# Optimization experiments

Hardware: AMD Instinct MI355X
Metric: run time of the kernel (lower is better)

## Reference

```python
import jax, jax.numpy as jnp
import numpy as np
from jax import lax

B = 64          # graphs per batch
N0 = 1024       # nodes per graph (equal-sized graphs -> static topk shapes)
DEG = 16        # avg degree
E = B * N0 * DEG
D_IN, D_H, D_OUT = 100, 128, 256
RATIO, EPS = 0.5, 1e-5


def _seg_sum(v, idx, n):
    return jax.ops.segment_sum(v, idx, num_segments=n)


def _gcn(x, src, dst, w_e, W, b, n):
    h = x @ W
    deg = 1.0 + _seg_sum(w_e, dst, n)          # +1 for self-loop
    dinv = lax.rsqrt(deg)
    norm = (dinv[src] * dinv[dst] * w_e)[:, None]
    return _seg_sum(h[src] * norm, dst, n) + h / deg[:, None] + b


def _graphnorm(x, w, bias, ms, nb, k):
    # PyG GraphNorm: per-graph mean/var with learnable mean_scale
    xg = x.reshape(nb, k, -1)
    mean = xg.mean(1, keepdims=True)
    sub = xg - ms * mean
    var = (sub * sub).mean(1, keepdims=True)
    return (w * sub * lax.rsqrt(var + EPS) + bias).reshape(nb * k, -1)


def _topk(x, src, dst, emask, p, nb, n_per):
    # TopKPooling (min_score=None): score = tanh(x.p/||p||), keep top ceil(r*n)
    k = int(np.ceil(RATIO * n_per))
    score = jnp.tanh((x @ p) / jnp.linalg.norm(p))
    vals, idx = lax.top_k(score.reshape(nb, n_per), k)            # [nb, k]
    perm = (idx + (jnp.arange(nb) * n_per)[:, None]).reshape(-1)
    x_new = x[perm] * vals.reshape(-1)[:, None]
    mapping = jnp.full((nb * n_per,), -1, jnp.int32).at[perm].set(
        jnp.arange(nb * k, dtype=jnp.int32))
    ns, nd = mapping[src], mapping[dst]
    valid = emask & (ns >= 0) & (nd >= 0)   # filter_adj as a persistent mask
    return x_new, jnp.where(valid, ns, 0), jnp.where(valid, nd, 0), valid, k


def _forward(x, edge_index, W1, b1, W2, b2, W3, b3,
             gn1_w, gn1_b, gn1_ms, gn2_w, gn2_b, gn2_ms,
             gn3_w, gn3_b, gn3_ms, p1, p2, p3):
    src, dst = edge_index[0], edge_index[1]
    emask = jnp.ones(src.shape, bool)
    Ws, bs = (W1, W2, W3), (b1, b2, b3)
    gw = (gn1_w, gn2_w, gn3_w)
    gb = (gn1_b, gn2_b, gn3_b)
    gm = (gn1_ms, gn2_ms, gn3_ms)
    ps = (p1, p2, p3)
    n_per = N0
    for i in range(3):
        n = B * n_per
        x = _gcn(x, src, dst, emask.astype(x.dtype), Ws[i], bs[i], n)
        x = _graphnorm(x, gw[i], gb[i], gm[i], B, n_per)
        x = jax.nn.relu(x)              # dropout: identity in eval mode
        x, src, dst, emask, n_per = _topk(x, src, dst, emask, ps[i], B, n_per)
    xg = x.reshape(B, n_per, D_OUT)
    # global mean/max pool then concat -> [B, 2*D_OUT]
    return jnp.concatenate([xg.mean(1), xg.max(1)], axis=1)


def setup_inputs():
    key = jax.random.key(0)
    ks = jax.random.split(key, 20)
    x = jax.random.normal(ks[0], (B * N0, D_IN), jnp.float32)
    # random edges within each graph, then offset by graph base index
    e = jax.random.randint(ks[1], (2, B, N0 * DEG), 0, N0, jnp.int32)
    edge_index = (e + (jnp.arange(B, dtype=jnp.int32) * N0)[None, :, None]).reshape(2, -1)
    batch = jnp.repeat(jnp.arange(B, dtype=jnp.int32), N0)
    inp = dict(x=x, edge_index=edge_index, batch=batch)
    dims = [(D_IN, D_H), (D_H, D_H), (D_H, D_OUT)]
    for i, (di, do) in enumerate(dims, 1):
        inp[f"W{i}"] = jax.random.normal(ks[1 + i], (di, do), jnp.float32) / np.sqrt(di)
        inp[f"b{i}"] = jnp.zeros((do,), jnp.float32)
        inp[f"gn{i}_w"] = jnp.ones((do,), jnp.float32)
        inp[f"gn{i}_b"] = jnp.zeros((do,), jnp.float32)
        inp[f"gn{i}_ms"] = jnp.ones((do,), jnp.float32)
        inp[f"p{i}"] = jax.random.normal(ks[10 + i], (do,), jnp.float32)
    return inp


def reference(x, edge_index, batch, W1, b1, W2, b2, W3, b3,
              gn1_w, gn1_b, gn1_ms, gn2_w, gn2_b, gn2_ms,
              gn3_w, gn3_b, gn3_ms, p1, p2, p3):
    del batch  # equal-sized graphs: grouping is encoded by constants B, N0
    return _forward(x, edge_index, W1, b1, W2, b2, W3, b3,
                    gn1_w, gn1_b, gn1_ms, gn2_w, gn2_b, gn2_ms,
                    gn3_w, gn3_b, gn3_ms, p1, p2, p3)
```

## Files before the change

### kernel.cpp

```cpp
#include <hip/hip_runtime.h>

#define GN_EPS 1e-5f

constexpr int NB   = 64;
constexpr int EPG  = 16384;
constexpr int ETOT = NB * EPG;
constexpr int NTOT = 64 * 1024;

__global__ void cmap_init_kernel(int* __restrict__ cmap) {
    int i = blockIdx.x * blockDim.x + threadIdx.x;
    if (i < NTOT) cmap[i] = i;
}

template <int NPG>
__global__ __launch_bounds__(1024) void csr_build_kernel(
        const int* __restrict__ ei, const int* __restrict__ cmap,
        int* __restrict__ cnt, int* __restrict__ offs, float* __restrict__ dinv,
        int2* __restrict__ csr_pack) {
    __shared__ int   lcnt[NPG];
    __shared__ float sdv[NPG];
    __shared__ int   wsum[16];
    constexpr int NW = NPG / 64;
    const int g = blockIdx.x;
    const int t = threadIdx.x;
    const int ebase = g * EPG;
    constexpr int EPT = EPG / 1024;

    for (int i = t; i < NPG; i += 1024) lcnt[i] = 0;
    __syncthreads();

    int ms_[EPT], md_[EPT];
#pragma unroll
    for (int i = 0; i < EPT; i++) {
        int e = ebase + t + i * 1024;
        int s = cmap[ei[e]];
        int d = cmap[ei[ETOT + e]];
        bool ok = (s >= 0) && (d >= 0);
        ms_[i] = ok ? s : -1;
        md_[i] = ok ? (d - g * NPG) : 0;
        if (ok) atomicAdd(&lcnt[d - g * NPG], 1);
    }
    __syncthreads();

    const int lane = t & 63;
    const int wid  = t >> 6;
    int orig = (t < NPG) ? lcnt[t] : 0;
    int v = orig;
#pragma unroll
    for (int d = 1; d < 64; d <<= 1) {
        int u = __shfl_up(v, d);
        if (lane >= d) v += u;
    }
    if (lane == 63) wsum[wid] = v;
    __syncthreads();
    if (wid == 0) {
        int wv = (lane < NW) ? wsum[lane] : 0;
#pragma unroll
        for (int d = 1; d < 16; d <<= 1) {
            int u = __shfl_up(wv, d);
            if (lane >= d) wv += u;
        }
        if (lane < NW) wsum[lane] = wv;
    }
    __syncthreads();
    if (t < NPG) {
        int incl = v + ((wid > 0) ? wsum[wid - 1] : 0);
        int excl = incl - orig;
        float dv = rsqrtf(1.0f + (float)orig);
        cnt[g * NPG + t]  = orig;
        offs[g * NPG + t] = ebase + excl;
        dinv[g * NPG + t] = dv;
        sdv[t] = dv;
        lcnt[t] = excl;
    }
    __syncthreads();

#pragma unroll
    for (int i = 0; i < EPT; i++) {
        int s = ms_[i];
        if (s >= 0) {
            int pos = atomicAdd(&lcnt[md_[i]], 1);
            csr_pack[ebase + pos] = make_int2(s, __float_as_int(sdv[s - g * NPG]));
        }
    }
}

template <int D4>
__global__ __launch_bounds__(256) void gather_kernel(
        const float* __restrict__ x, const int* __restrict__ cnt,
        const int* __restrict__ offs, const float* __restrict__ dinv,
        const int2* __restrict__ csr_pack, float* __restrict__ z, int n, int bpg) {
    constexpr int GRP = 8;
    constexpr int NPB = 256 / GRP;
    constexpr int CPL = 4;
    int bid   = blockIdx.x;
    int xcd   = bid & 7;
    int slot  = bid >> 3;
    int graph = xcd + 8 * (slot / bpg);
    int local = slot % bpg;
    int vb    = graph * bpg + local;

    int grp  = threadIdx.x / GRP;
    int lane = threadIdx.x % GRP;
    int v = vb * NPB + grp;
    if (v >= n) return;

    const float4* x4 = reinterpret_cast<const float4*>(x);
    int st = offs[v];
    int c  = cnt[v];
    float dv = dinv[v];

    int f4_[CPL];
    bool act[CPL];
#pragma unroll
    for (int i = 0; i < CPL; i++) {
        f4_[i] = lane + GRP * i;
        act[i] = f4_[i] < D4;
    }

    float4 acc[CPL];
#pragma unroll
    for (int i = 0; i < CPL; i++) {
        if (act[i]) {
            float4 xv = x4[(size_t)v * D4 + f4_[i]];
            acc[i] = {xv.x * dv, xv.y * dv, xv.z * dv, xv.w * dv};
        } else {
            acc[i] = {0.f, 0.f, 0.f, 0.f};
        }
    }

    int j = 0;
    for (; j + 2 <= c; j += 2) {
        int2 p0 = csr_pack[st + j];
        int2 p1 = csr_pack[st + j + 1];
        float d0 = __int_as_float(p0.y);
        float d1 = __int_as_float(p1.y);
        size_t r0 = (size_t)p0.x * D4;
        size_t r1 = (size_t)p1.x * D4;
#pragma unroll
        for (int i = 0; i < CPL; i++) {
            if (!act[i]) continue;
            float4 h0 = x4[r0 + f4_[i]];
            float4 h1 = x4[r1 + f4_[i]];
            acc[i].x += h0.x * d0 + h1.x * d1;
            acc[i].y += h0.y * d0 + h1.y * d1;
            acc[i].z += h0.z * d0 + h1.z * d1;
            acc[i].w += h0.w * d0 + h1.w * d1;
        }
    }
    if (j < c) {
        int2 p0 = csr_pack[st + j];
        float d0 = __int_as_float(p0.y);
        size_t r0 = (size_t)p0.x * D4;
#pragma unroll
        for (int i = 0; i < CPL; i++) {
            if (!act[i]) continue;
            float4 h0 = x4[r0 + f4_[i]];
            acc[i].x += h0.x * d0; acc[i].y += h0.y * d0;
            acc[i].z += h0.z * d0; acc[i].w += h0.w * d0;
        }
    }
#pragma unroll
    for (int i = 0; i < CPL; i++) {
        if (!act[i]) continue;
        float4 o = {acc[i].x * dv, acc[i].y * dv, acc[i].z * dv, acc[i].w * dv};
        reinterpret_cast<float4*>(z)[(size_t)v * D4 + f4_[i]] = o;
    }
}

__global__ __launch_bounds__(256) void gemm128_kernel(const float* __restrict__ A,
                                                      const float* __restrict__ W,
                                                      const float* __restrict__ Bias,
                                                      float* __restrict__ C,
                                                      int M, int N, int K) {
    __shared__ float As[16][132];
    __shared__ float Bs[16][132];
    const int bm = blockIdx.x * 128;
    const int bn = blockIdx.y * 128;
    const int tid = threadIdx.x;
    const int tx = tid & 15, ty = tid >> 4;

    const int arow = tid >> 1;
    const int ak   = (tid & 1) * 8;
    const int brow = tid >> 5;
    const int bc4  = (tid & 31) * 4;

    float acc[2][2][4][4] = {};

    for (int k0 = 0; k0 < K; k0 += 16) {
        {
            const float* ap = A + (size_t)(bm + arow) * K + k0 + ak;
            float4 a0 = {0,0,0,0}, a1 = {0,0,0,0};
            if (k0 + ak < K)     a0 = *reinterpret_cast<const float4*>(ap);
            if (k0 + ak + 4 < K) a1 = *reinterpret_cast<const float4*>(ap + 4);
            As[ak + 0][arow] = a0.x; As[ak + 1][arow] = a0.y;
            As[ak + 2][arow] = a0.z; As[ak + 3][arow] = a0.w;
            As[ak + 4][arow] = a1.x; As[ak + 5][arow] = a1.y;
            As[ak + 6][arow] = a1.z; As[ak + 7][arow] = a1.w;
        }
        {
            float4 b0 = {0,0,0,0}, b1 = {0,0,0,0};
            if (k0 + brow < K)
                b0 = *reinterpret_cast<const float4*>(W + (size_t)(k0 + brow) * N + bn + bc4);
            if (k0 + brow + 8 < K)
                b1 = *reinterpret_cast<const float4*>(W + (size_t)(k0 + brow + 8) * N + bn + bc4);
            *reinterpret_cast<float4*>(&Bs[brow][bc4])     = b0;
            *reinterpret_cast<float4*>(&Bs[brow + 8][bc4]) = b1;
        }
        __syncthreads();
#pragma unroll
        for (int k = 0; k < 16; k++) {
            float4 a0 = *reinterpret_cast<const float4*>(&As[k][ty * 4]);
            float4 a1 = *reinterpret_cast<const float4*>(&As[k][64 + ty * 4]);
            float4 b0 = *reinterpret_cast<const float4*>(&Bs[k][tx * 4]);
            float4 b1 = *reinterpret_cast<const float4*>(&Bs[k][64 + tx * 4]);
            const float av[2][4] = {{a0.x, a0.y, a0.z, a0.w}, {a1.x, a1.y, a1.z, a1.w}};
            const float bv[2][4] = {{b0.x, b0.y, b0.z, b0.w}, {b1.x, b1.y, b1.z, b1.w}};
#pragma unroll
            for (int qi = 0; qi < 2; qi++)
#pragma unroll
                for (int qj = 0; qj < 2; qj++)
#pragma unroll
                    for (int i = 0; i < 4; i++)
#pragma unroll
                        for (int j = 0; j < 4; j++)
                            acc[qi][qj][i][j] += av[qi][i] * bv[qj][j];
        }
        __syncthreads();
    }
    float4 bb[2];
    bb[0] = *reinterpret_cast<const float4*>(&Bias[bn + tx * 4]);
    bb[1] = *reinterpret_cast<const float4*>(&Bias[bn + 64 + tx * 4]);
#pragma unroll
    for (int qi = 0; qi < 2; qi++)
#pragma unroll
        for (int i = 0; i < 4; i++) {
            int row = bm + qi * 64 + ty * 4 + i;
#pragma unroll
            for (int qj = 0; qj < 2; qj++) {
                float4 o = {acc[qi][qj][i][0] + bb[qj].x, acc[qi][qj][i][1] + bb[qj].y,
                            acc[qi][qj][i][2] + bb[qj].z, acc[qi][qj][i][3] + bb[qj].w};
                *reinterpret_cast<float4*>(&C[(size_t)row * N + bn + qj * 64 + tx * 4]) = o;
            }
        }
}

template <int D4>
__global__ __launch_bounds__(256) void gn_partial_kernel(
        const float* __restrict__ x, float* __restrict__ sum1, float* __restrict__ sum2,
        int n_per) {
    constexpr int GROUPS = 256 / D4;
    __shared__ float4 l1[256];
    __shared__ float4 l2[256];
    int g = blockIdx.x >> 3;
    int ch = blockIdx.x & 7;
    int f4 = threadIdx.x % D4;
    int grp = threadIdx.x / D4;
    int chunk = n_per / 8;
    int base = g * n_per + ch * chunk;
    const float4* x4 = reinterpret_cast<const float4*>(x);
    float4 s1 = {0.f, 0.f, 0.f, 0.f}, s2 = {0.f, 0.f, 0.f, 0.f};
    for (int i = grp; i < chunk; i += GROUPS) {
        float4 v = x4[(size_t)(base + i) * D4 + f4];
        s1.x += v.x; s1.y += v.y; s1.z += v.z; s1.w += v.w;
        s2.x += v.x * v.x; s2.y += v.y * v.y; s2.z += v.z * v.z; s2.w += v.w * v.w;
    }
    int t = threadIdx.x;
    l1[t] = s1; l2[t] = s2;
    __syncthreads();
    for (int str = 128; str >= D4; str >>= 1) {
        if (t < str) {
            float4 a = l1[t + str], b2 = l2[t + str];
            l1[t].x += a.x; l1[t].y += a.y; l1[t].z += a.z; l1[t].w += a.w;
            l2[t].x += b2.x; l2[t].y += b2.y; l2[t].z += b2.z; l2[t].w += b2.w;
        }
        __syncthreads();
    }
    if (t < D4) {
        size_t slot = (size_t)(g * 8 + ch) * (D4 * 4) + t * 4;
        *reinterpret_cast<float4*>(&sum1[slot]) = l1[t];
        *reinterpret_cast<float4*>(&sum2[slot]) = l2[t];
    }
}

__global__ void pnorm3_kernel(const float* __restrict__ p0, const float* __restrict__ p1,
                              const float* __restrict__ p2, int d0, int d1, int d2,
                              float* __restrict__ out) {
    __shared__ float red[256];
    const float* p = (blockIdx.x == 0) ? p0 : (blockIdx.x == 1) ? p1 : p2;
    int d          = (blockIdx.x == 0) ? d0 : (blockIdx.x == 1) ? d1 : d2;
    int t = threadIdx.x;
    float v = (t < d) ? p[t] : 0.0f;
    red[t] = v * v;
    __syncthreads();
    for (int s = 128; s; s >>= 1) {
        if (t < s) red[t] += red[t + s];
        __syncthreads();
    }
    if (t == 0) out[blockIdx.x] = 1.0f / sqrtf(red[0]);
}

template <int DO>
__global__ __launch_bounds__(256) void gn_apply_score_kernel(
        float* __restrict__ x, const float* __restrict__ sum1, const float* __restrict__ sum2,
        const float* __restrict__ ms, const float* __restrict__ w,
        const float* __restrict__ bias, const float* __restrict__ p,
        const float* __restrict__ pinv, float* __restrict__ score, int n_per) {
    constexpr int V = DO / 64;
    __shared__ float scm[DO];
    __shared__ float ssr[DO];
    int node = blockIdx.x * 4 + (threadIdx.x >> 6);
    int lane = threadIdx.x & 63;
    int g = node / n_per;
    float inv_n = 1.0f / (float)n_per;
    for (int f = threadIdx.x; f < DO; f += 256) {
        float s1 = 0.f, s2 = 0.f;
#pragma unroll
        for (int ch = 0; ch < 8; ch++) {
            s1 += sum1[(size_t)(g * 8 + ch) * DO + f];
            s2 += sum2[(size_t)(g * 8 + ch) * DO + f];
        }
        float mean = s1 * inv_n;
        float ex2  = s2 * inv_n;
        float m = ms[f];
        float var = ex2 - 2.f * m * mean * mean + m * m * mean * mean;
        scm[f] = m * mean;
        ssr[f] = w[f] * rsqrtf(var + GN_EPS);
    }
    __syncthreads();

    float*       xr = x + (size_t)node * DO + lane * V;
    const float* bb = bias + lane * V;
    const float* pp = p + lane * V;
    float dot = 0.f;
#pragma unroll
    for (int i = 0; i < V; i++) {
        int f = lane * V + i;
        float y = (xr[i] - scm[f]) * ssr[f] + bb[i];
        y = fmaxf(y, 0.0f);
        xr[i] = y;
        dot += y * pp[i];
    }
#pragma unroll
    for (int off = 32; off; off >>= 1) dot += __shfl_xor(dot, off);
    if (lane == 0) score[node] = tanhf(dot * pinv[0]);
}

template <int N, int K>
__global__ __launch_bounds__(1024) void topk_radix_kernel(
        const float* __restrict__ score, int* __restrict__ mapping,
        int* __restrict__ inv) {
    __shared__ int hist[256];
    __shared__ int sscan[N];
    __shared__ int sbyte, sneed;
    const int g = blockIdx.x;
    const int t = threadIdx.x;
    float sc = score[g * N + t];
    unsigned u = __float_as_uint(sc);
    unsigned key = (u & 0x80000000u) ? ~u : (u | 0x80000000u);

    unsigned prefix = 0;
    int need = K;
#pragma unroll
    for (int shift = 24; shift >= 0; shift -= 8) {
        if (t < 256) hist[t] = 0;
        __syncthreads();
        unsigned hm = (shift == 24) ? 0u : (0xFFFFFFFFu << (shift + 8));
        if ((key & hm) == (prefix & hm))
            atomicAdd(&hist[(key >> shift) & 255], 1);
        __syncthreads();
        if (t < 256) sscan[t] = hist[t];
        __syncthreads();
        for (int d = 1; d < 256; d <<= 1) {
            int x = (t < 256 && t + d < 256) ? sscan[t + d] : 0;
            __syncthreads();
            if (t < 256) sscan[t] += x;
            __syncthreads();
        }
        if (t < 256) {
            int ge  = sscan[t];
            int gt_ = (t + 1 < 256) ? sscan[t + 1] : 0;
            if (ge >= need && gt_ < need) { sbyte = t; sneed = need - gt_; }
        }
        __syncthreads();
        prefix |= ((unsigned)sbyte << shift);
        need = sneed;
        __syncthreads();
    }
    bool gt = key > prefix;
    bool eq = (key == prefix);
    sscan[t] = (gt ? (1 << 16) : 0) | (eq ? 1 : 0);
    __syncthreads();
    for (int d = 1; d < N; d <<= 1) {
        int x = (t >= d) ? sscan[t - d] : 0;
        __syncthreads();
        sscan[t] += x;
        __syncthreads();
    }
    int incl   = sscan[t];
    int gtrank = (incl >> 16) - (gt ? 1 : 0);
    int eqrank = (incl & 0xFFFF) - (eq ? 1 : 0);
    int cntGT  = K - need;
    bool sel = gt || (eq && (eqrank < need));
    int old_g = g * N + t;
    if (sel) {
        int slot = gt ? gtrank : (cntGT + eqrank);
        mapping[old_g] = g * K + slot;
        inv[g * K + slot] = old_g;
    } else {
        mapping[old_g] = -1;
    }
}

__global__ void permute_compose_kernel(const float* __restrict__ x, const int* __restrict__ inv,
                                       const float* __restrict__ score, float* __restrict__ xn,
                                       int total, int ldof4,
                                       int* __restrict__ cmap, const int* __restrict__ mapping) {
    int t = blockIdx.x * blockDim.x + threadIdx.x;
    if (t < total) {
        int node = t >> ldof4;
        int f4   = t & ((1 << ldof4) - 1);
        int dof4 = 1 << ldof4;
        int old = inv[node];
        float sc = score[old];
        float4 v = reinterpret_cast<const float4*>(x)[(size_t)old * dof4 + f4];
        float4 o = {v.x * sc, v.y * sc, v.z * sc, v.w * sc};
        reinterpret_cast<float4*>(xn)[t] = o;
    }
    if (t < NTOT) {
        int c = cmap[t];
        cmap[t] = (c >= 0) ? mapping[c] : -1;
    }
}

__global__ __launch_bounds__(1024) void pool_sel_kernel(const float* __restrict__ x,
                                                        const int* __restrict__ inv,
                                                        const float* __restrict__ score,
                                                        float* __restrict__ out) {
    __shared__ float ssum[1024];
    __shared__ float smax[1024];
    int g = blockIdx.x;
    int f = threadIdx.x & 255;
    int ch = threadIdx.x >> 8;
    float s = 0.f, mx = -INFINITY;
    for (int i = ch; i < 128; i += 4) {
        int old = inv[g * 128 + i];
        float sc = score[old];
        float v = x[(size_t)old * 256 + f] * sc;
        s += v;
        mx = fmaxf(mx, v);
    }
    ssum[threadIdx.x] = s;
    smax[threadIdx.x] = mx;
    __syncthreads();
    if (ch == 0) {
#pragma unroll
        for (int c = 1; c < 4; c++) {
            s  += ssum[f + c * 256];
            mx  = fmaxf(mx, smax[f + c * 256]);
        }
        out[g * 512 + f]       = s / 128.0f;
        out[g * 512 + 256 + f] = mx;
    }
}

static inline int cdiv_h(int a, int b) { return (a + b - 1) / b; }

extern "C" void kernel_launch(void* const* d_in, const int* in_sizes, int n_in,
                              void* d_out, int out_size, void* d_ws, size_t ws_size,
                              hipStream_t stream) {
    (void)in_sizes; (void)n_in; (void)out_size; (void)ws_size;

    const float* x_in = (const float*)d_in[0];
    const int*   ei   = (const int*)d_in[1];
    const float* Wm[3]  = {(const float*)d_in[3],  (const float*)d_in[9],  (const float*)d_in[15]};
    const float* bv[3]  = {(const float*)d_in[4],  (const float*)d_in[10], (const float*)d_in[16]};
    const float* gnw[3] = {(const float*)d_in[5],  (const float*)d_in[11], (const float*)d_in[17]};
    const float* gnb[3] = {(const float*)d_in[6],  (const float*)d_in[12], (const float*)d_in[18]};
    const float* gnm[3] = {(const float*)d_in[7],  (const float*)d_in[13], (const float*)d_in[19]};
    const float* pv[3]  = {(const float*)d_in[8],  (const float*)d_in[14], (const float*)d_in[20]};

    size_t off = 0;
    auto alloc = [&](size_t bytes) {
        void* p = (char*)d_ws + off;
        off += (bytes + 255) & ~(size_t)255;
        return p;
    };
    float* X1      = (float*)alloc((size_t)65536 * 128 * 4);
    float* Z       = (float*)alloc((size_t)65536 * 128 * 4);
    float* X2      = (float*)alloc((size_t)32768 * 128 * 4);
    int2*  csr_pack= (int2*)alloc((size_t)ETOT * 8);
    int*   cmap    = (int*)alloc(NTOT * 4);
    int*   cnt     = (int*)alloc(65536 * 4);
    int*   offs    = (int*)alloc(65536 * 4);
    float* dinv    = (float*)alloc(65536 * 4);
    float* score   = (float*)alloc(65536 * 4);
    int*   mapping = (int*)alloc(65536 * 4);
    int*   inv     = (int*)alloc(32768 * 4);
    float* sum1    = (float*)alloc(64 * 8 * 256 * 4);
    float* sum2    = (float*)alloc(64 * 8 * 256 * 4);
    float* pinv    = (float*)alloc(256);

    const int nper[4] = {1024, 512, 256, 128};
    const int din[3]  = {100, 128, 128};
    const int dof[3]  = {128, 128, 256};

    cmap_init_kernel<<<NTOT / 256, 256, 0, stream>>>(cmap);
    pnorm3_kernel<<<3, 256, 0, stream>>>(pv[0], pv[1], pv[2], dof[0], dof[1], dof[2], pinv);

    for (int L = 0; L < 3; L++) {
        const int n    = NB * nper[L];
        const int k    = nper[L + 1];
        const int nn   = NB * k;
        const int D    = dof[L];
        const int dof4 = D / 4;
        const int ldof4 = (dof4 == 32) ? 5 : 6;
        const float* xin = (L == 0) ? x_in : X2;

        if (nper[L] == 1024)
            csr_build_kernel<1024><<<NB, 1024, 0, stream>>>(ei, cmap, cnt, offs, dinv, csr_pack);
        else if (nper[L] == 512)
            csr_build_kernel<512><<<NB, 1024, 0, stream>>>(ei, cmap, cnt, offs, dinv, csr_pack);
        else
            csr_build_kernel<256><<<NB, 1024, 0, stream>>>(ei, cmap, cnt, offs, dinv, csr_pack);

        {
            const int NPB = 32;
            const int bpg = nper[L] / NPB;
            if (L == 0)
                gather_kernel<25><<<n / NPB, 256, 0, stream>>>(xin, cnt, offs, dinv,
                                                               csr_pack, Z, n, bpg);
            else
                gather_kernel<32><<<n / NPB, 256, 0, stream>>>(xin, cnt, offs, dinv,
                                                               csr_pack, Z, n, bpg);
        }

        gemm128_kernel<<<dim3(n / 128, D / 128), 256, 0, stream>>>(Z, Wm[L], bv[L], X1,
                                                                   n, D, din[L]);

        if (dof4 == 32)
            gn_partial_kernel<32><<<NB * 8, 256, 0, stream>>>(X1, sum1, sum2, nper[L]);
        else
            gn_partial_kernel<64><<<NB * 8, 256, 0, stream>>>(X1, sum1, sum2, nper[L]);

        if (D == 128)
            gn_apply_score_kernel<128><<<n / 4, 256, 0, stream>>>(X1, sum1, sum2, gnm[L],
                                                                  gnw[L], gnb[L], pv[L],
                                                                  pinv + L, score, nper[L]);
        else
            gn_apply_score_kernel<256><<<n / 4, 256, 0, stream>>>(X1, sum1, sum2, gnm[L],
                                                                  gnw[L], gnb[L], pv[L],
                                                                  pinv + L, score, nper[L]);

        if (nper[L] == 1024)
            topk_radix_kernel<1024, 512><<<NB, 1024, 0, stream>>>(score, mapping, inv);
        else if (nper[L] == 512)
            topk_radix_kernel<512, 256><<<NB, 512, 0, stream>>>(score, mapping, inv);
        else
            topk_radix_kernel<256, 128><<<NB, 256, 0, stream>>>(score, mapping, inv);

        if (L < 2) {
            int total = nn * dof4;
            permute_compose_kernel<<<cdiv_h(total, 256), 256, 0, stream>>>(
                X1, inv, score, X2, total, ldof4, cmap, mapping);
        } else {
            pool_sel_kernel<<<NB, 1024, 0, stream>>>(X1, inv, score, (float*)d_out);
        }
    }
}
```

Measured before the change: 315.0 us.

## Fuse GraphNorm partial sums into GEMM epilogue and unroll gather by four

```diff
diff --git a/kernel.cpp b/kernel.cpp
--- a/kernel.cpp
+++ b/kernel.cpp
@@ -129,26 +129,36 @@
         }
     }
 
-    int j = 0;
-    for (; j + 2 <= c; j += 2) {
-        int2 p0 = csr_pack[st + j];
-        int2 p1 = csr_pack[st + j + 1];
-        float d0 = __int_as_float(p0.y);
-        float d1 = __int_as_float(p1.y);
-        size_t r0 = (size_t)p0.x * D4;
-        size_t r1 = (size_t)p1.x * D4;
+    const int nfull = c & ~3;
+    int2 pk[4];
+    if (nfull > 0) {
+#pragma unroll
+        for (int u = 0; u < 4; u++) pk[u] = csr_pack[st + u];
+    }
+    for (int j = 0; j < nfull; j += 4) {
+        int2 cur0 = pk[0], cur1 = pk[1], cur2 = pk[2], cur3 = pk[3];
+        if (j + 8 <= nfull) {
+#pragma unroll
+            for (int u = 0; u < 4; u++) pk[u] = csr_pack[st + j + 4 + u];
+        }
+        float d0 = __int_as_float(cur0.y), d1 = __int_as_float(cur1.y);
+        float d2 = __int_as_float(cur2.y), d3 = __int_as_float(cur3.y);
+        size_t r0 = (size_t)cur0.x * D4, r1 = (size_t)cur1.x * D4;
+        size_t r2 = (size_t)cur2.x * D4, r3 = (size_t)cur3.x * D4;
 #pragma unroll
         for (int i = 0; i < CPL; i++) {
             if (!act[i]) continue;
             float4 h0 = x4[r0 + f4_[i]];
             float4 h1 = x4[r1 + f4_[i]];
-            acc[i].x += h0.x * d0 + h1.x * d1;
-            acc[i].y += h0.y * d0 + h1.y * d1;
-            acc[i].z += h0.z * d0 + h1.z * d1;
-            acc[i].w += h0.w * d0 + h1.w * d1;
-        }
-    }
-    if (j < c) {
+            float4 h2 = x4[r2 + f4_[i]];
+            float4 h3 = x4[r3 + f4_[i]];
+            acc[i].x += h0.x * d0 + h1.x * d1 + h2.x * d2 + h3.x * d3;
+            acc[i].y += h0.y * d0 + h1.y * d1 + h2.y * d2 + h3.y * d3;
+            acc[i].z += h0.z * d0 + h1.z * d1 + h2.z * d2 + h3.z * d3;
+            acc[i].w += h0.w * d0 + h1.w * d1 + h2.w * d2 + h3.w * d3;
+        }
+    }
+    for (int j = nfull; j < c; j++) {
         int2 p0 = csr_pack[st + j];
         float d0 = __int_as_float(p0.y);
         size_t r0 = (size_t)p0.x * D4;
@@ -172,9 +182,13 @@
                                                       const float* __restrict__ W,
                                                       const float* __restrict__ Bias,
                                                       float* __restrict__ C,
-                                                      int M, int N, int K) {
+                                                      float* __restrict__ sum1,
+                                                      float* __restrict__ sum2,
+                                                      int M, int N, int K, int nper) {
     __shared__ float As[16][132];
     __shared__ float Bs[16][132];
+    __shared__ float red1[4][132];
+    __shared__ float red2[4][132];
     const int bm = blockIdx.x * 128;
     const int bn = blockIdx.y * 128;
     const int tid = threadIdx.x;
@@ -231,6 +245,8 @@
     float4 bb[2];
     bb[0] = *reinterpret_cast<const float4*>(&Bias[bn + tx * 4]);
     bb[1] = *reinterpret_cast<const float4*>(&Bias[bn + 64 + tx * 4]);
+
+    float s1l[2][4] = {}, s2l[2][4] = {};
 #pragma unroll
     for (int qi = 0; qi < 2; qi++)
 #pragma unroll
@@ -238,48 +254,47 @@
             int row = bm + qi * 64 + ty * 4 + i;
 #pragma unroll
             for (int qj = 0; qj < 2; qj++) {
-                float4 o = {acc[qi][qj][i][0] + bb[qj].x, acc[qi][qj][i][1] + bb[qj].y,
-                            acc[qi][qj][i][2] + bb[qj].z, acc[qi][qj][i][3] + bb[qj].w};
+                float o0 = acc[qi][qj][i][0] + bb[qj].x;
+                float o1 = acc[qi][qj][i][1] + bb[qj].y;
+                float o2 = acc[qi][qj][i][2] + bb[qj].z;
+                float o3 = acc[qi][qj][i][3] + bb[qj].w;
+                float4 o = {o0, o1, o2, o3};
                 *reinterpret_cast<float4*>(&C[(size_t)row * N + bn + qj * 64 + tx * 4]) = o;
+                s1l[qj][0] += o0; s2l[qj][0] += o0 * o0;
+                s1l[qj][1] += o1; s2l[qj][1] += o1 * o1;
+                s1l[qj][2] += o2; s2l[qj][2] += o2 * o2;
+                s1l[qj][3] += o3; s2l[qj][3] += o3 * o3;
             }
         }
-}
-
-template <int D4>
-__global__ __launch_bounds__(256) void gn_partial_kernel(
-        const float* __restrict__ x, float* __restrict__ sum1, float* __restrict__ sum2,
-        int n_per) {
-    constexpr int GROUPS = 256 / D4;
-    __shared__ float4 l1[256];
-    __shared__ float4 l2[256];
-    int g = blockIdx.x >> 3;
-    int ch = blockIdx.x & 7;
-    int f4 = threadIdx.x % D4;
-    int grp = threadIdx.x / D4;
-    int chunk = n_per / 8;
-    int base = g * n_per + ch * chunk;
-    const float4* x4 = reinterpret_cast<const float4*>(x);
-    float4 s1 = {0.f, 0.f, 0.f, 0.f}, s2 = {0.f, 0.f, 0.f, 0.f};
-    for (int i = grp; i < chunk; i += GROUPS) {
-        float4 v = x4[(size_t)(base + i) * D4 + f4];
-        s1.x += v.x; s1.y += v.y; s1.z += v.z; s1.w += v.w;
-        s2.x += v.x * v.x; s2.y += v.y * v.y; s2.z += v.z * v.z; s2.w += v.w * v.w;
-    }
-    int t = threadIdx.x;
-    l1[t] = s1; l2[t] = s2;
-    __syncthreads();
-    for (int str = 128; str >= D4; str >>= 1) {
-        if (t < str) {
-            float4 a = l1[t + str], b2 = l2[t + str];
-            l1[t].x += a.x; l1[t].y += a.y; l1[t].z += a.z; l1[t].w += a.w;
-            l2[t].x += b2.x; l2[t].y += b2.y; l2[t].z += b2.z; l2[t].w += b2.w;
-        }
-        __syncthreads();
-    }
-    if (t < D4) {
-        size_t slot = (size_t)(g * 8 + ch) * (D4 * 4) + t * 4;
-        *reinterpret_cast<float4*>(&sum1[slot]) = l1[t];
-        *reinterpret_cast<float4*>(&sum2[slot]) = l2[t];
+    const int wv = tid >> 6;
+#pragma unroll
+    for (int qj = 0; qj < 2; qj++)
+#pragma unroll
+        for (int j = 0; j < 4; j++) {
+            float v1 = s1l[qj][j], v2 = s2l[qj][j];
+            v1 += __shfl_xor(v1, 16); v1 += __shfl_xor(v1, 32);
+            v2 += __shfl_xor(v2, 16); v2 += __shfl_xor(v2, 32);
+            if ((tid & 48) == 0) {
+                red1[wv][tx * 8 + qj * 4 + j] = v1;
+                red2[wv][tx * 8 + qj * 4 + j] = v2;
+            }
+        }
+    __syncthreads();
+    if (tid < 16) {
+        const int g   = bm / nper;
+        const int nch = nper >> 7;
+        const int ch  = (bm % nper) >> 7;
+        size_t slotbase = (size_t)(g * nch + ch) * N + bn;
+#pragma unroll
+        for (int qj = 0; qj < 2; qj++)
+#pragma unroll
+            for (int j = 0; j < 4; j++) {
+                int k = tid * 8 + qj * 4 + j;
+                float v1 = red1[0][k] + red1[1][k] + red1[2][k] + red1[3][k];
+                float v2 = red2[0][k] + red2[1][k] + red2[2][k] + red2[3][k];
+                sum1[slotbase + qj * 64 + tid * 4 + j] = v1;
+                sum2[slotbase + qj * 64 + tid * 4 + j] = v2;
+            }
     }
 }
 
@@ -305,7 +320,7 @@
         float* __restrict__ x, const float* __restrict__ sum1, const float* __restrict__ sum2,
         const float* __restrict__ ms, const float* __restrict__ w,
         const float* __restrict__ bias, const float* __restrict__ p,
-        const float* __restrict__ pinv, float* __restrict__ score, int n_per) {
+        const float* __restrict__ pinv, float* __restrict__ score, int n_per, int nch) {
     constexpr int V = DO / 64;
     __shared__ float scm[DO];
     __shared__ float ssr[DO];
@@ -315,10 +330,9 @@
     float inv_n = 1.0f / (float)n_per;
     for (int f = threadIdx.x; f < DO; f += 256) {
         float s1 = 0.f, s2 = 0.f;
-#pragma unroll
-        for (int ch = 0; ch < 8; ch++) {
-            s1 += sum1[(size_t)(g * 8 + ch) * DO + f];
-            s2 += sum2[(size_t)(g * 8 + ch) * DO + f];
+        for (int ch = 0; ch < nch; ch++) {
+            s1 += sum1[(size_t)(g * nch + ch) * DO + f];
+            s2 += sum2[(size_t)(g * nch + ch) * DO + f];
         }
         float mean = s1 * inv_n;
         float ex2  = s2 * inv_n;
@@ -515,6 +529,7 @@
         const int D    = dof[L];
         const int dof4 = D / 4;
         const int ldof4 = (dof4 == 32) ? 5 : 6;
+        const int nch  = nper[L] / 128;
         const float* xin = (L == 0) ? x_in : X2;
 
         if (nper[L] == 1024)
@@ -536,21 +551,17 @@
         }
 
         gemm128_kernel<<<dim3(n / 128, D / 128), 256, 0, stream>>>(Z, Wm[L], bv[L], X1,
-                                                                   n, D, din[L]);
-
-        if (dof4 == 32)
-            gn_partial_kernel<32><<<NB * 8, 256, 0, stream>>>(X1, sum1, sum2, nper[L]);
-        else
-            gn_partial_kernel<64><<<NB * 8, 256, 0, stream>>>(X1, sum1, sum2, nper[L]);
+                                                                   sum1, sum2,
+                                                                   n, D, din[L], nper[L]);
 
         if (D == 128)
             gn_apply_score_kernel<128><<<n / 4, 256, 0, stream>>>(X1, sum1, sum2, gnm[L],
                                                                   gnw[L], gnb[L], pv[L],
-                                                                  pinv + L, score, nper[L]);
+                                                                  pinv + L, score, nper[L], nch);
         else
             gn_apply_score_kernel<256><<<n / 4, 256, 0, stream>>>(X1, sum1, sum2, gnm[L],
                                                                   gnw[L], gnb[L], pv[L],
-                                                                  pinv + L, score, nper[L]);
+                                                                  pinv + L, score, nper[L], nch);
 
         if (nper[L] == 1024)
             topk_radix_kernel<1024, 512><<<NB, 1024, 0, stream>>>(score, mapping, inv);
```

Result: no change. 316.3 us (+0.4%).
